# Kernel tuning notes

Hardware: AMD Instinct MI355X
Metric: run time of the kernel (lower is better)

Reference implementation:

```python
import jax, jax.numpy as jnp
import numpy as np

C = 256          # channels
G = 16           # dcn groups
K = 3            # dcn kernel size (P = K*K sampling points)
PAD = 1
DIL = 1
OFFSET_SCALE = 1.0
HIDDEN = 4 * C   # mlp_ratio = 4
EPS = 1e-6


def layer_norm(x, g, b):
    mu = x.mean(-1, keepdims=True)
    var = jnp.mean((x - mu) ** 2, -1, keepdims=True)
    return (x - mu) * jax.lax.rsqrt(var + EPS) * g + b


def grid_sample_bilinear(img, grid):
    """img: (B,Cg,H,W); grid: (B,L,P,2) xy in [-1,1].
    Matches F.grid_sample(mode='bilinear', padding_mode='zeros', align_corners=False)."""
    B, Cg, H, W = img.shape
    x = (grid[..., 0] + 1.0) * (W * 0.5) - 0.5
    y = (grid[..., 1] + 1.0) * (H * 0.5) - 0.5
    x0f = jnp.floor(x); y0f = jnp.floor(y)
    wx1 = x - x0f; wy1 = y - y0f
    x0 = x0f.astype(jnp.int32); y0 = y0f.astype(jnp.int32)
    flat = img.reshape(B, Cg, H * W)

    def tap(ix, iy, w):
        valid = (ix >= 0) & (ix < W) & (iy >= 0) & (iy < H)
        idx = jnp.clip(iy, 0, H - 1) * W + jnp.clip(ix, 0, W - 1)
        v = jnp.take_along_axis(flat, idx.reshape(B, 1, -1), axis=2)
        v = v.reshape(B, Cg, idx.shape[1], idx.shape[2])
        return v * (w * valid)[:, None]

    return (tap(x0, y0, (1 - wx1) * (1 - wy1))
            + tap(x0 + 1, y0, wx1 * (1 - wy1))
            + tap(x0, y0 + 1, (1 - wx1) * wy1)
            + tap(x0 + 1, y0 + 1, wx1 * wy1))


def dcnv3(x, dw_w, dw_b, off_w, off_b, mask_w, mask_b, inp_w, inp_b, out_w, out_b):
    """DCNv3 forward (dcnv3_core_pytorch math), x: (N,H,W,C) channels_last."""
    N, H, W, Cc = x.shape
    Cg = Cc // G
    P = K * K
    xp = x @ inp_w.T + inp_b                             # input_proj
    x1 = jax.lax.conv_general_dilated(
        x, dw_w, (1, 1), [(PAD, PAD), (PAD, PAD)],
        dimension_numbers=('NHWC', 'HWIO', 'NHWC'),
        feature_group_count=Cc) + dw_b                   # depthwise conv
    off = (x1 @ off_w.T + off_b).reshape(N, H, W, G, P, 2)
    m = jax.nn.softmax((x1 @ mask_w.T + mask_b).reshape(N, H, W, G, P), axis=-1)
    Hin, Win = H + 2 * PAD, W + 2 * PAD
    xpad = jnp.pad(xp, ((0, 0), (PAD, PAD), (PAD, PAD), (0, 0)))
    base = (DIL * (K - 1)) // 2
    ry = (jnp.arange(H, dtype=x.dtype) * 1.0 + base + 0.5) / Hin
    rx = (jnp.arange(W, dtype=x.dtype) * 1.0 + base + 0.5) / Win
    ref = jnp.stack([jnp.broadcast_to(rx[None, :], (H, W)),
                     jnp.broadcast_to(ry[:, None], (H, W))], -1)   # (H,W,2) xy
    xs = (jnp.arange(K, dtype=x.dtype) * DIL - base) / Win
    ys = (jnp.arange(K, dtype=x.dtype) * DIL - base) / Hin
    gx, gy = jnp.meshgrid(xs, ys, indexing='ij')         # w-major order as in torch ref
    grid = jnp.stack([gx, gy], -1).reshape(P, 2)
    norm = jnp.array([Win, Hin], dtype=x.dtype)
    loc = (ref[None, :, :, None, None, :] + grid * OFFSET_SCALE
           + off * (OFFSET_SCALE / norm))                # (N,H,W,G,P,2)
    sg = 2.0 * loc - 1.0
    img = xpad.reshape(N, Hin, Win, G, Cg).transpose(0, 3, 4, 1, 2).reshape(N * G, Cg, Hin, Win)
    sgr = sg.transpose(0, 3, 1, 2, 4, 5).reshape(N * G, H * W, P, 2)
    sampled = grid_sample_bilinear(img, sgr)             # (N*G,Cg,HW,P)
    mr = m.transpose(0, 3, 1, 2, 4).reshape(N * G, 1, H * W, P)
    out = (sampled * mr).sum(-1).reshape(N, G, Cg, H * W)
    out = out.transpose(0, 3, 1, 2).reshape(N, H, W, Cc)
    return out @ out_w.T + out_b                         # output_proj


def setup_inputs() -> dict:
    key = jax.random.key(0)
    ks = jax.random.split(key, 10)
    N, H, W = 8, 56, 56
    P = K * K

    def rn(k, shape, s):
        return jax.random.normal(k, shape, dtype=jnp.float32) * s

    return {
        'x': jax.random.normal(ks[0], (N, H, W, C), dtype=jnp.float32),
        'ln1_g': jnp.ones((C,), jnp.float32), 'ln1_b': jnp.zeros((C,), jnp.float32),
        'dw_w': rn(ks[1], (K, K, 1, C), 0.1), 'dw_b': jnp.zeros((C,), jnp.float32),
        'off_w': rn(ks[2], (G * P * 2, C), 0.02), 'off_b': jnp.zeros((G * P * 2,), jnp.float32),
        'mask_w': rn(ks[3], (G * P, C), 0.02), 'mask_b': jnp.zeros((G * P,), jnp.float32),
        'inp_w': rn(ks[4], (C, C), 0.05), 'inp_b': jnp.zeros((C,), jnp.float32),
        'out_w': rn(ks[5], (C, C), 0.05), 'out_b': jnp.zeros((C,), jnp.float32),
        'ln2_g': jnp.ones((C,), jnp.float32), 'ln2_b': jnp.zeros((C,), jnp.float32),
        'fc1_w': rn(ks[6], (HIDDEN, C), 0.05), 'fc1_b': jnp.zeros((HIDDEN,), jnp.float32),
        'fc2_w': rn(ks[7], (C, HIDDEN), 0.05), 'fc2_b': jnp.zeros((C,), jnp.float32),
    }


def reference(x, ln1_g, ln1_b, dw_w, dw_b, off_w, off_b, mask_w, mask_b,
              inp_w, inp_b, out_w, out_b, ln2_g, ln2_b, fc1_w, fc1_b, fc2_w, fc2_b):
    # pre-norm block, no layer_scale, drop_path=0
    y = x + dcnv3(layer_norm(x, ln1_g, ln1_b), dw_w, dw_b, off_w, off_b,
                  mask_w, mask_b, inp_w, inp_b, out_w, out_b)
    h = layer_norm(y, ln2_g, ln2_b)
    h = jax.nn.gelu(h @ fc1_w.T + fc1_b, approximate=False)
    return y + (h @ fc2_w.T + fc2_b)
```

## Files before the change

kernel.cpp:

```cpp
#include <hip/hip_runtime.h>
#include <hip/hip_bf16.h>
#include <math.h>

#define NTOK 25088
#define HW_  3136
#define HH   56
#define WW   56
#define CCH  256
#define NGRP 16
#define NPTS 9
#define HIDN 1024
#define NOFFM 432
#define TPB  4

typedef __attribute__((ext_vector_type(8))) __bf16 bf16x8;
typedef __attribute__((ext_vector_type(4))) __bf16 bf16x4;
typedef __attribute__((ext_vector_type(4))) float  f32x4;

static __device__ __forceinline__ void gl_lds16(const void* g, void* l) {
    __builtin_amdgcn_global_load_lds((const __attribute__((address_space(1))) void*)g,
                                     (__attribute__((address_space(3))) void*)l, 16, 0, 0);
}

static __device__ __forceinline__ float gelu_fast(float v) {
    float z = 0.7978845608028654f * (v + 0.044715f * v * v * v);
    float t = 1.0f - 2.0f / (__expf(2.0f * z) + 1.0f);
    return 0.5f * v * (1.0f + t);
}

__global__ __launch_bounds__(256)
void cvt_all_kernel(const float* __restrict__ inp_w, const float* __restrict__ out_w,
                    const float* __restrict__ off_w, const float* __restrict__ mask_w,
                    const float* __restrict__ fc1_w, const float* __restrict__ fc2_w,
                    __bf16* wib, __bf16* wob, __bf16* wcat, __bf16* w1b, __bf16* w2b) {
    int i = blockIdx.x * 256 + threadIdx.x;
    const float* s; __bf16* d; int off;
    if (i < 16384)       { s = inp_w;  d = wib;          off = i; }
    else if (i < 32768)  { s = out_w;  d = wob;          off = i - 16384; }
    else if (i < 51200)  { s = off_w;  d = wcat;         off = i - 32768; }
    else if (i < 60416)  { s = mask_w; d = wcat + 73728; off = i - 51200; }
    else if (i < 125952) { s = fc1_w;  d = w1b;          off = i - 60416; }
    else if (i < 191488) { s = fc2_w;  d = w2b;          off = i - 125952; }
    else return;
    float4 v = ((const float4*)s)[off];
    bf16x4 o = {(__bf16)v.x, (__bf16)v.y, (__bf16)v.z, (__bf16)v.w};
    ((bf16x4*)d)[off] = o;
}

__global__ void biascat_kernel(const float* __restrict__ ob, const float* __restrict__ mb,
                               float* __restrict__ bc) {
    int i = threadIdx.x;
    if (i < 288) bc[i] = ob[i];
    else if (i < 432) bc[i] = mb[i - 288];
}

__global__ __launch_bounds__(256)
void ln_kernel(const float* __restrict__ x, const float* __restrict__ g,
               const float* __restrict__ b, __bf16* __restrict__ outb, int ntok) {
    int gid  = blockIdx.x * 256 + threadIdx.x;
    int t    = gid >> 6;
    int lane = threadIdx.x & 63;
    if (t >= ntok) return;
    float4 v = ((const float4*)(x + (size_t)t * CCH))[lane];
    float s = v.x + v.y + v.z + v.w;
#pragma unroll
    for (int o = 1; o < 64; o <<= 1) s += __shfl_xor(s, o);
    float mu = s * 0.00390625f;
    float dx = v.x - mu, dy = v.y - mu, dz = v.z - mu, dw = v.w - mu;
    float q = dx * dx + dy * dy + dz * dz + dw * dw;
#pragma unroll
    for (int o = 1; o < 64; o <<= 1) q += __shfl_xor(q, o);
    float rstd = rsqrtf(q * 0.00390625f + 1e-6f);
    float4 gg = ((const float4*)g)[lane];
    float4 bb = ((const float4*)b)[lane];
    bf16x4 ob = {(__bf16)(dx * rstd * gg.x + bb.x), (__bf16)(dy * rstd * gg.y + bb.y),
                 (__bf16)(dz * rstd * gg.z + bb.z), (__bf16)(dw * rstd * gg.w + bb.w)};
    ((bf16x4*)(outb + (size_t)t * CCH))[lane] = ob;
}

__global__ __launch_bounds__(256)
void dwconv_kernel(const __bf16* __restrict__ ln, const float* __restrict__ wt,
                   const float* __restrict__ bias, __bf16* __restrict__ out) {
    int gid = blockIdx.x * 256 + threadIdx.x;
    int t = gid >> 6;
    int cq = gid & 63;
    if (t >= NTOK) return;
    int n = t / HW_, hw = t % HW_;
    int h = hw / WW, w0 = hw % WW;
    float4 a = ((const float4*)bias)[cq];
    const bf16x4* l4 = (const bf16x4*)ln;
    const float4* w4 = (const float4*)wt;
#pragma unroll
    for (int ky = 0; ky < 3; ++ky) {
        int y = h + ky - 1;
        if (y < 0 || y >= HH) continue;
#pragma unroll
        for (int kx = 0; kx < 3; ++kx) {
            int x = w0 + kx - 1;
            if (x < 0 || x >= WW) continue;
            bf16x4 v = l4[(size_t)(n * HW_ + y * WW + x) * 64 + cq];
            float4 ww = w4[(ky * 3 + kx) * 64 + cq];
            a.x += (float)v[0] * ww.x; a.y += (float)v[1] * ww.y;
            a.z += (float)v[2] * ww.z; a.w += (float)v[3] * ww.w;
        }
    }
    bf16x4 ob = {(__bf16)a.x, (__bf16)a.y, (__bf16)a.z, (__bf16)a.w};
    ((bf16x4*)out)[(size_t)t * 64 + cq] = ob;
}

template <int EPI>
__global__ __launch_bounds__(256, 4)
void gemm_kernel(const __bf16* __restrict__ A, const __bf16* __restrict__ W,
                 const float* __restrict__ bias, const float* __restrict__ resid,
                 float* __restrict__ outf, __bf16* __restrict__ outb,
                 const int Ndim, const int Kdim) {
    __shared__ __align__(16) __bf16 Alds[128 * 32];
    __shared__ __align__(16) __bf16 Blds[128 * 32];

    const int tid  = threadIdx.x;
    const int w    = tid >> 6;
    const int lane = tid & 63;
    const int m0   = blockIdx.x * 128;
    const int n0   = blockIdx.y * 128;
    const int wr   = (w >> 1) * 64;
    const int wc   = (w & 1) * 64;

    f32x4 acc[4][4];
#pragma unroll
    for (int i = 0; i < 4; ++i)
#pragma unroll
        for (int j = 0; j < 4; ++j) acc[i][j] = (f32x4){0.f, 0.f, 0.f, 0.f};

    const int c0 = (w * 2 + 0) * 64 + lane;
    const int c1 = (w * 2 + 1) * 64 + lane;
    const int ar0 = c0 >> 2, ab0 = ((c0 & 3) ^ ((c0 >> 4) & 3)) * 16;
    const int ar1 = c1 >> 2, ab1 = ((c1 & 3) ^ ((c1 >> 4) & 3)) * 16;
    int br0 = n0 + ar0; if (br0 > Ndim - 1) br0 = Ndim - 1;
    int br1 = n0 + ar1; if (br1 > Ndim - 1) br1 = Ndim - 1;

    const char* Ab = (const char*)A;
    const char* Wb = (const char*)W;
    char* AL = (char*)Alds;
    char* BL = (char*)Blds;
    const size_t rb = (size_t)Kdim * 2;

    const int mrow = lane & 15;
    const int q    = lane >> 4;
    const int kA   = ((q ^ (mrow >> 2)) & 3) * 16;
    const int kB   = ((q ^ mrow) & 3) * 16;

    for (int k0 = 0; k0 < Kdim; k0 += 32) {
        const size_t kb = (size_t)k0 * 2;
        gl_lds16(Ab + (size_t)(m0 + ar0) * rb + kb + ab0, AL + (w * 2 + 0) * 1024);
        gl_lds16(Ab + (size_t)(m0 + ar1) * rb + kb + ab1, AL + (w * 2 + 1) * 1024);
        gl_lds16(Wb + (size_t)br0 * rb + kb + ab0,        BL + (w * 2 + 0) * 1024);
        gl_lds16(Wb + (size_t)br1 * rb + kb + ab1,        BL + (w * 2 + 1) * 1024);
        __syncthreads();
        bf16x8 af[4], bfr[4];
#pragma unroll
        for (int i = 0; i < 4; ++i)
            af[i] = *(const bf16x8*)(AL + (wr + i * 16 + mrow) * 64 + kA);
#pragma unroll
        for (int i = 0; i < 4; ++i)
            bfr[i] = *(const bf16x8*)(BL + (wc + 4 * mrow + i) * 64 + kB);
#pragma unroll
        for (int mi = 0; mi < 4; ++mi)
#pragma unroll
            for (int ni = 0; ni < 4; ++ni)
                acc[mi][ni] = __builtin_amdgcn_mfma_f32_16x16x32_bf16(af[mi], bfr[ni], acc[mi][ni], 0, 0, 0);
        __syncthreads();
    }

    const int coll = lane & 15;
    const int rowh = (lane >> 4) * 4;
    const int col0 = n0 + wc + 4 * coll;
    if (col0 < Ndim) {
        const float4 bv = *(const float4*)(bias + col0);
#pragma unroll
        for (int mi = 0; mi < 4; ++mi) {
#pragma unroll
            for (int j = 0; j < 4; ++j) {
                const int row = m0 + wr + mi * 16 + rowh + j;
                const size_t idx = (size_t)row * (size_t)Ndim + col0;
                float4 v = make_float4(acc[mi][0][j] + bv.x, acc[mi][1][j] + bv.y,
                                       acc[mi][2][j] + bv.z, acc[mi][3][j] + bv.w);
                if (EPI == 1) {
                    const float4 r = *(const float4*)(resid + idx);
                    v.x += r.x; v.y += r.y; v.z += r.z; v.w += r.w;
                    *(float4*)(outf + idx) = v;
                } else if (EPI == 2) {
                    bf16x4 ob = {(__bf16)gelu_fast(v.x), (__bf16)gelu_fast(v.y),
                                 (__bf16)gelu_fast(v.z), (__bf16)gelu_fast(v.w)};
                    *(bf16x4*)(outb + idx) = ob;
                } else {
                    bf16x4 ob = {(__bf16)v.x, (__bf16)v.y, (__bf16)v.z, (__bf16)v.w};
                    *(bf16x4*)(outb + idx) = ob;
                }
            }
        }
    }
}

__global__ __launch_bounds__(256)
void dcn_kernel(const __bf16* __restrict__ xp, const __bf16* __restrict__ om,
                __bf16* __restrict__ out) {
    __shared__ float  raw[TPB][NOFFM];
    __shared__ int4   sidx[NPTS][TPB * NGRP];
    __shared__ float4 swt[NPTS][TPB * NGRP];
    const int tid = threadIdx.x;
    const int bid = blockIdx.x;
    const int b   = (bid & 7) * 784 + (bid >> 3);
    const int t0  = b * TPB;

    if (tid < (TPB * NOFFM) / 8) {
        bf16x8 v = *(const bf16x8*)(om + (size_t)t0 * NOFFM + tid * 8);
        float* d = &raw[0][0] + tid * 8;
#pragma unroll
        for (int k = 0; k < 8; ++k) d[k] = (float)v[k];
    }
    __syncthreads();

    if (tid < TPB * NGRP) {
        const int lt = tid >> 4, g = tid & 15;
        float* m = &raw[lt][288 + g * 9];
        float mx = m[0];
#pragma unroll
        for (int p = 1; p < 9; ++p) mx = fmaxf(mx, m[p]);
        float s = 0.f, e[9];
#pragma unroll
        for (int p = 0; p < 9; ++p) { e[p] = __expf(m[p] - mx); s += e[p]; }
        const float inv = 1.f / s;
#pragma unroll
        for (int p = 0; p < 9; ++p) m[p] = e[p] * inv;
    }
    __syncthreads();

    for (int e = tid; e < TPB * NGRP * NPTS; e += 256) {
        const int lt = e / 144, r = e % 144, g = r / 9, p = r % 9;
        const int t  = t0 + lt;
        const int hw = t % HW_;
        const int h = hw / WW, w0 = hw % WW;
        const float offx = raw[lt][g * 18 + p * 2 + 0];
        const float offy = raw[lt][g * 18 + p * 2 + 1];
        const float pm   = raw[lt][288 + g * 9 + p];
        const int kx = p / 3, ky = p % 3;
        const float fx = (float)(w0 + kx - 1) + offx;
        const float fy = (float)(h  + ky - 1) + offy;
        const float x0f = floorf(fx), y0f = floorf(fy);
        const float wx = fx - x0f, wy = fy - y0f;
        const int x0 = (int)x0f, y0 = (int)y0f;
        const bool xv0 = (unsigned)x0 < WW, xv1 = (unsigned)(x0 + 1) < WW;
        const bool yv0 = (unsigned)y0 < HH, yv1 = (unsigned)(y0 + 1) < HH;
        const int xc0 = min(max(x0, 0), WW - 1), xc1 = min(max(x0 + 1, 0), WW - 1);
        const int yc0 = min(max(y0, 0), HH - 1), yc1 = min(max(y0 + 1, 0), HH - 1);
        const int tg = lt * 16 + g;
        sidx[p][tg] = make_int4(yc0 * WW + xc0, yc0 * WW + xc1, yc1 * WW + xc0, yc1 * WW + xc1);
        swt[p][tg]  = make_float4((xv0 && yv0) ? (1.f - wx) * (1.f - wy) * pm : 0.f,
                                  (xv1 && yv0) ? wx * (1.f - wy) * pm : 0.f,
                                  (xv0 && yv1) ? (1.f - wx) * wy * pm : 0.f,
                                  (xv1 && yv1) ? wx * wy * pm : 0.f);
    }
    __syncthreads();

    const int lt = tid >> 6, lane = tid & 63;
    const int g = lane >> 2;
    const int t = t0 + lt;
    const int n = t / HW_;
    const int tg = lt * 16 + g;
    const __bf16* base = xp + (size_t)n * HW_ * CCH + lane * 4;
    f32x4 acc = {0.f, 0.f, 0.f, 0.f};
#pragma unroll
    for (int p = 0; p < NPTS; ++p) {
        const int4   id = sidx[p][tg];
        const float4 wv = swt[p][tg];
        bf16x4 v0 = *(const bf16x4*)(base + (size_t)id.x * CCH);
        bf16x4 v1 = *(const bf16x4*)(base + (size_t)id.y * CCH);
        bf16x4 v2 = *(const bf16x4*)(base + (size_t)id.z * CCH);
        bf16x4 v3 = *(const bf16x4*)(base + (size_t)id.w * CCH);
#pragma unroll
        for (int k = 0; k < 4; ++k)
            acc[k] += wv.x * (float)v0[k] + wv.y * (float)v1[k]
                    + wv.z * (float)v2[k] + wv.w * (float)v3[k];
    }
    bf16x4 ob = {(__bf16)acc[0], (__bf16)acc[1], (__bf16)acc[2], (__bf16)acc[3]};
    ((bf16x4*)out)[(size_t)t * 64 + lane] = ob;
}

extern "C" void kernel_launch(void* const* d_in, const int* in_sizes, int n_in,
                              void* d_out, int out_size, void* d_ws, size_t ws_size,
                              hipStream_t stream) {
    const float* x      = (const float*)d_in[0];
    const float* ln1_g  = (const float*)d_in[1];
    const float* ln1_b  = (const float*)d_in[2];
    const float* dw_w   = (const float*)d_in[3];
    const float* dw_b   = (const float*)d_in[4];
    const float* off_w  = (const float*)d_in[5];
    const float* off_b  = (const float*)d_in[6];
    const float* mask_w = (const float*)d_in[7];
    const float* mask_b = (const float*)d_in[8];
    const float* inp_w  = (const float*)d_in[9];
    const float* inp_b  = (const float*)d_in[10];
    const float* out_w  = (const float*)d_in[11];
    const float* out_b  = (const float*)d_in[12];
    const float* ln2_g  = (const float*)d_in[13];
    const float* ln2_b  = (const float*)d_in[14];
    const float* fc1_w  = (const float*)d_in[15];
    const float* fc1_b  = (const float*)d_in[16];
    const float* fc2_w  = (const float*)d_in[17];
    const float* fc2_b  = (const float*)d_in[18];
    float* out = (float*)d_out;

    char* ws = (char*)d_ws;
    size_t o = 0;
    auto alloc = [&](size_t bytes) { size_t r = o; o += (bytes + 255) & ~(size_t)255; return r; };
    float*  yf    = (float*)(ws + alloc((size_t)NTOK * CCH * 4));
    __bf16* x1b   = (__bf16*)(ws + alloc((size_t)NTOK * CCH * 2));
    __bf16* lnb   = (__bf16*)(ws + alloc((size_t)NTOK * CCH * 2));
    __bf16* xpb   = (__bf16*)(ws + alloc((size_t)NTOK * CCH * 2));
    __bf16* offmb = (__bf16*)(ws + alloc((size_t)NTOK * NOFFM * 2));
    alloc(4 * 1024 * 1024);
    __bf16* wib   = (__bf16*)(ws + alloc((size_t)65536 * 2));
    __bf16* wob   = (__bf16*)(ws + alloc((size_t)65536 * 2));
    __bf16* wcat  = (__bf16*)(ws + alloc((size_t)110592 * 2));
    __bf16* w1b   = (__bf16*)(ws + alloc((size_t)262144 * 2));
    __bf16* w2b   = (__bf16*)(ws + alloc((size_t)262144 * 2));
    float*  bcat  = (float*)(ws + alloc((size_t)432 * 4));
    if (ws_size < o) return;

    __bf16* dcnb = lnb;
    __bf16* l2b  = x1b;
    __bf16* h1b  = lnb;

    cvt_all_kernel<<<748, 256, 0, stream>>>(inp_w, out_w, off_w, mask_w, fc1_w, fc2_w,
                                            wib, wob, wcat, w1b, w2b);
    biascat_kernel<<<1, 512, 0, stream>>>(off_b, mask_b, bcat);

    ln_kernel<<<NTOK / 4, 256, 0, stream>>>(x, ln1_g, ln1_b, lnb, NTOK);
    dwconv_kernel<<<NTOK / 4, 256, 0, stream>>>(lnb, dw_w, dw_b, x1b);
    gemm_kernel<3><<<dim3(196, 4), 256, 0, stream>>>(x1b, wcat, bcat, nullptr, nullptr, offmb, NOFFM, 256);
    gemm_kernel<3><<<dim3(196, 2), 256, 0, stream>>>(lnb, wib, inp_b, nullptr, nullptr, xpb, 256, 256);
    dcn_kernel<<<NTOK / TPB, 256, 0, stream>>>(xpb, offmb, dcnb);
    gemm_kernel<1><<<dim3(196, 2), 256, 0, stream>>>(dcnb, wob, out_b, x, yf, nullptr, 256, 256);
    ln_kernel<<<NTOK / 4, 256, 0, stream>>>(yf, ln2_g, ln2_b, l2b, NTOK);
    gemm_kernel<2><<<dim3(196, 8), 256, 0, stream>>>(l2b, w1b, fc1_b, nullptr, nullptr, h1b, 1024, 256);
    gemm_kernel<1><<<dim3(196, 2), 256, 0, stream>>>(h1b, w2b, fc2_b, yf, out, nullptr, 256, 1024);
}
```

Baseline: 196.6 us.

## Double-buffer GEMM LDS tiles and remap B rows for conflict-free reads

The GEMM kernel now keeps two LDS buffers for the A and B tiles. It issues the global-to-LDS loads for the next K slice before running the MFMAs on the current one, so there is one barrier per iteration instead of two. The B tile row permutation and XOR swizzle are also remapped so each lane reads contiguous 16-row groups instead of stride-4 rows, which should reduce LDS bank conflicts. LDS use per block doubles, which may lower occupancy under launch_bounds(256,4).

```diff
diff --git a/kernel.cpp b/kernel.cpp
--- a/kernel.cpp
+++ b/kernel.cpp
@@ -114,8 +114,8 @@
                  const float* __restrict__ bias, const float* __restrict__ resid,
                  float* __restrict__ outf, __bf16* __restrict__ outb,
                  const int Ndim, const int Kdim) {
-    __shared__ __align__(16) __bf16 Alds[128 * 32];
-    __shared__ __align__(16) __bf16 Blds[128 * 32];
+    __shared__ __align__(16) __bf16 Alds[2][128 * 32];
+    __shared__ __align__(16) __bf16 Blds[2][128 * 32];
 
     const int tid  = threadIdx.x;
     const int w    = tid >> 6;
@@ -131,45 +131,67 @@
 #pragma unroll
         for (int j = 0; j < 4; ++j) acc[i][j] = (f32x4){0.f, 0.f, 0.f, 0.f};
 
-    const int c0 = (w * 2 + 0) * 64 + lane;
-    const int c1 = (w * 2 + 1) * 64 + lane;
-    const int ar0 = c0 >> 2, ab0 = ((c0 & 3) ^ ((c0 >> 4) & 3)) * 16;
-    const int ar1 = c1 >> 2, ab1 = ((c1 & 3) ^ ((c1 >> 4) & 3)) * 16;
-    int br0 = n0 + ar0; if (br0 > Ndim - 1) br0 = Ndim - 1;
-    int br1 = n0 + ar1; if (br1 > Ndim - 1) br1 = Ndim - 1;
+    const int p0 = (w * 2 + 0) * 64 + lane;
+    const int p1 = p0 + 64;
+    const int ar0 = p0 >> 2, ab0 = ((p0 & 3) ^ ((p0 >> 4) & 3)) * 16;
+    const int ar1 = p1 >> 2, ab1 = ((p1 & 3) ^ ((p1 >> 4) & 3)) * 16;
+    const int br0 = p0 >> 2, br1 = p1 >> 2;
+    int bR0 = n0 + ((br0 >> 6) << 6) + 4 * (br0 & 15) + ((br0 >> 4) & 3);
+    int bR1 = n0 + ((br1 >> 6) << 6) + 4 * (br1 & 15) + ((br1 >> 4) & 3);
+    if (bR0 > Ndim - 1) bR0 = Ndim - 1;
+    if (bR1 > Ndim - 1) bR1 = Ndim - 1;
+    const int bb0 = ((p0 & 3) ^ ((p0 >> 3) & 3)) * 16;
+    const int bb1 = ((p1 & 3) ^ ((p1 >> 3) & 3)) * 16;
 
     const char* Ab = (const char*)A;
     const char* Wb = (const char*)W;
-    char* AL = (char*)Alds;
-    char* BL = (char*)Blds;
+    char* AL = (char*)&Alds[0][0];
+    char* BL = (char*)&Blds[0][0];
     const size_t rb = (size_t)Kdim * 2;
+    const size_t sA0 = (size_t)(m0 + ar0) * rb + ab0;
+    const size_t sA1 = (size_t)(m0 + ar1) * rb + ab1;
+    const size_t sB0 = (size_t)bR0 * rb + bb0;
+    const size_t sB1 = (size_t)bR1 * rb + bb1;
+    const int d0 = (w * 2 + 0) * 1024;
+    const int d1 = (w * 2 + 1) * 1024;
+
+#define STAGE(BUF, KB)                                        \
+    do {                                                      \
+        gl_lds16(Ab + sA0 + (KB), AL + (BUF) * 8192 + d0);    \
+        gl_lds16(Ab + sA1 + (KB), AL + (BUF) * 8192 + d1);    \
+        gl_lds16(Wb + sB0 + (KB), BL + (BUF) * 8192 + d0);    \
+        gl_lds16(Wb + sB1 + (KB), BL + (BUF) * 8192 + d1);    \
+    } while (0)
 
     const int mrow = lane & 15;
     const int q    = lane >> 4;
     const int kA   = ((q ^ (mrow >> 2)) & 3) * 16;
-    const int kB   = ((q ^ mrow) & 3) * 16;
-
+    const int kB   = ((q ^ (mrow >> 1)) & 3) * 16;
+
+    int cur = 0;
+    STAGE(0, 0);
+    __syncthreads();
     for (int k0 = 0; k0 < Kdim; k0 += 32) {
-        const size_t kb = (size_t)k0 * 2;
-        gl_lds16(Ab + (size_t)(m0 + ar0) * rb + kb + ab0, AL + (w * 2 + 0) * 1024);
-        gl_lds16(Ab + (size_t)(m0 + ar1) * rb + kb + ab1, AL + (w * 2 + 1) * 1024);
-        gl_lds16(Wb + (size_t)br0 * rb + kb + ab0,        BL + (w * 2 + 0) * 1024);
-        gl_lds16(Wb + (size_t)br1 * rb + kb + ab1,        BL + (w * 2 + 1) * 1024);
-        __syncthreads();
+        const bool more = (k0 + 32 < Kdim);
+        if (more) STAGE(cur ^ 1, (size_t)(k0 + 32) * 2);
         bf16x8 af[4], bfr[4];
 #pragma unroll
         for (int i = 0; i < 4; ++i)
-            af[i] = *(const bf16x8*)(AL + (wr + i * 16 + mrow) * 64 + kA);
+            af[i] = *(const bf16x8*)(AL + cur * 8192 + (wr + i * 16 + mrow) * 64 + kA);
 #pragma unroll
         for (int i = 0; i < 4; ++i)
-            bfr[i] = *(const bf16x8*)(BL + (wc + 4 * mrow + i) * 64 + kB);
+            bfr[i] = *(const bf16x8*)(BL + cur * 8192 + (wc + i * 16 + mrow) * 64 + kB);
 #pragma unroll
         for (int mi = 0; mi < 4; ++mi)
 #pragma unroll
             for (int ni = 0; ni < 4; ++ni)
                 acc[mi][ni] = __builtin_amdgcn_mfma_f32_16x16x32_bf16(af[mi], bfr[ni], acc[mi][ni], 0, 0, 0);
-        __syncthreads();
-    }
+        if (more) {
+            __syncthreads();
+            cur ^= 1;
+        }
+    }
+#undef STAGE
 
     const int coll = lane & 15;
     const int rowh = (lane >> 4) * 4;
```

Result: no change. 193.7 us (-1.5%).
